# Performance work log

Hardware: AMD Instinct MI355X
Metric: run time of the kernel (lower is better)

Reference implementation:

```python
import jax, jax.numpy as jnp
import numpy as np

N, IN, HID, OUT = 8192, 512, 256, 128

def setup_inputs() -> dict:
    key = jax.random.key(0)
    k1, k2, k3, k4 = jax.random.split(key, 4)
    adj = jax.random.uniform(k1, (N, N), dtype=jnp.float32)
    feature = jax.random.normal(k2, (N, IN), dtype=jnp.float32)
    W1 = jax.random.normal(k3, (IN, HID), dtype=jnp.float32) * (1.0 / np.sqrt(IN))
    b1 = jnp.zeros((HID,), dtype=jnp.float32)
    W2 = jax.random.normal(k4, (HID, OUT), dtype=jnp.float32) * (1.0 / np.sqrt(HID))
    b2 = jnp.zeros((OUT,), dtype=jnp.float32)
    return {"adj": adj, "feature": feature, "W1": W1, "b1": b1, "W2": W2, "b2": b2}

def reference(adj, feature, W1, b1, W2, b2):
    # GCN encoder: layer1 (relu) then layer2 (linear output)
    h = jax.nn.relu(adj @ (feature @ W1) + b1)   # [N, HID]
    h = adj @ (h @ W2) + b2                      # [N, OUT]
    # InnerProductDecoder: sigmoid(flatten(h @ h.T))
    logits = h @ h.T                             # [N, N]
    h_noise = jax.nn.sigmoid(logits.reshape(-1)) # [N*N]
    return (h_noise, h)
```

## Files before the change

kernel.cpp:

```cpp
#include <hip/hip_runtime.h>


#define KSPLIT 8

typedef __bf16 bf16x8_t __attribute__((ext_vector_type(8)));
typedef __bf16 bf16x4_t __attribute__((ext_vector_type(4)));
typedef float  f32x4_t  __attribute__((ext_vector_type(4)));

#define MFMA_BF16(a, b, c) __builtin_amdgcn_mfma_f32_16x16x32_bf16((a), (b), (c), 0, 0, 0)

__device__ __forceinline__ bf16x8_t cvt8(float4 u, float4 v) {
    bf16x8_t o;
    o[0] = (__bf16)u.x; o[1] = (__bf16)u.y; o[2] = (__bf16)u.z; o[3] = (__bf16)u.w;
    o[4] = (__bf16)v.x; o[5] = (__bf16)v.y; o[6] = (__bf16)v.z; o[7] = (__bf16)v.w;
    return o;
}

__device__ __forceinline__ void gload_lds16(const void* g, void* l) {
    __builtin_amdgcn_global_load_lds(
        (const __attribute__((address_space(1))) unsigned int*)g,
        (__attribute__((address_space(3))) unsigned int*)l, 16, 0, 0);
}

__global__ __launch_bounds__(256) void cast_adj(
    const float* __restrict__ adj, __bf16* __restrict__ ab)
{
    const size_t j = (size_t)blockIdx.x * 256 + threadIdx.x;
    const float4* p = (const float4*)adj + j * 2;
    float4 u = p[0], v = p[1];
    *(bf16x8_t*)(ab + j * 8) = cvt8(u, v);
}

__global__ __launch_bounds__(256) void cast_all(
    const float* __restrict__ feat, const float* __restrict__ W1,
    const float* __restrict__ W2, __bf16* __restrict__ fb,
    __bf16* __restrict__ w1t, __bf16* __restrict__ w2t)
{
    const int j = blockIdx.x * 256 + threadIdx.x;
    if (j < 524288) {
        const float4* p = (const float4*)feat + (size_t)j * 2;
        float4 u = p[0], v = p[1];
        *(bf16x8_t*)(fb + (size_t)j * 8) = cvt8(u, v);
    } else if (j < 524288 + 131072) {
        int t = j - 524288;
        int k = t >> 8, n = t & 255;
        w1t[n * 512 + k] = (__bf16)W1[t];
    } else if (j < 524288 + 131072 + 32768) {
        int t = j - 655360;
        int k = t >> 7, n = t & 127;
        w2t[n * 256 + k] = (__bf16)W2[t];
    }
}

template<int MT, int WC>
__global__ __launch_bounds__(256, 2) void gemm_bt_cbf16(
    const __bf16* __restrict__ X, const __bf16* __restrict__ Yb,
    __bf16* __restrict__ C, int K, int N)
{
    constexpr int WR = 4 / WC;
    constexpr int BM = WR * MT * 16;
    constexpr int BN = WC * 64;
    const int mblk = blockIdx.x, nblk = blockIdx.y;
    const int w = threadIdx.x >> 6, lane = threadIdx.x & 63;
    const int wr = w / WC, wc = w % WC;
    const int q = lane >> 4, l16 = lane & 15;
    const int mbase = mblk * BM + wr * (MT * 16);
    const int nbase = nblk * BN + wc * 64;

    f32x4_t acc[MT][4];
    const f32x4_t z = {0.f, 0.f, 0.f, 0.f};
#pragma unroll
    for (int i = 0; i < MT; i++)
#pragma unroll
        for (int jj = 0; jj < 4; jj++) acc[i][jj] = z;

    const __bf16* Xr[MT];
    const __bf16* Yr[4];
#pragma unroll
    for (int i = 0; i < MT; i++) Xr[i] = X + (size_t)(mbase + i * 16 + l16) * K + q * 8;
#pragma unroll
    for (int jj = 0; jj < 4; jj++) Yr[jj] = Yb + (size_t)(nbase + jj * 16 + l16) * K + q * 8;

    for (int k = 0; k < K; k += 32) {
        bf16x8_t a[MT], b[4];
#pragma unroll
        for (int i = 0; i < MT; i++) a[i] = *(const bf16x8_t*)(Xr[i] + k);
#pragma unroll
        for (int jj = 0; jj < 4; jj++) b[jj] = *(const bf16x8_t*)(Yr[jj] + k);
#pragma unroll
        for (int i = 0; i < MT; i++)
#pragma unroll
            for (int jj = 0; jj < 4; jj++) acc[i][jj] = MFMA_BF16(a[i], b[jj], acc[i][jj]);
    }

#pragma unroll
    for (int i = 0; i < MT; i++)
#pragma unroll
        for (int jj = 0; jj < 4; jj++) {
            const int row0 = mbase + i * 16 + q * 4;
            const int col = nbase + jj * 16 + l16;
#pragma unroll
            for (int r = 0; r < 4; r++)
                C[(size_t)(row0 + r) * N + col] = (__bf16)acc[i][jj][r];
        }
}

template<int NN>
__global__ __launch_bounds__(256, 2) void gemm_adj_bf(
    const __bf16* __restrict__ A, const __bf16* __restrict__ Y,
    float* __restrict__ P, int kchunk)
{
    constexpr int NT = NN / 64;
    __shared__ __bf16 As[2][4096];

    const int mblk = blockIdx.x;
    const int ks = blockIdx.y;
    const int w = threadIdx.x >> 6, lane = threadIdx.x & 63;
    const int q = lane >> 4, l16 = lane & 15;
    const int kbase = ks * kchunk;
    const int ntiles = kchunk >> 6;

    const __bf16* gsrc[2];
    int loff[2];
#pragma unroll
    for (int j = 0; j < 2; j++) {
        const int row = j * 32 + w * 8 + (lane >> 3);
        const int gdst = lane & 7;
        const int gsrcg = gdst ^ (row & 7);
        gsrc[j] = A + (size_t)(mblk * 64 + row) * 8192 + kbase + gsrcg * 8;
        loff[j] = row * 64 + gdst * 8;
    }

    const __bf16* Yr[NT];
#pragma unroll
    for (int jj = 0; jj < NT; jj++)
        Yr[jj] = Y + (size_t)(w * (NN / 4) + jj * 16 + l16) * 8192 + q * 8;

    f32x4_t acc[4][NT];
    const f32x4_t z = {0.f, 0.f, 0.f, 0.f};
#pragma unroll
    for (int i = 0; i < 4; i++)
#pragma unroll
        for (int jj = 0; jj < NT; jj++) acc[i][jj] = z;

#pragma unroll
    for (int j = 0; j < 2; j++) gload_lds16(gsrc[j], &As[0][0] + loff[j]);

    int buf = 0;
    for (int kt = 0; kt < ntiles; kt++) {
        const int kk = kbase + (kt << 6);

        bf16x8_t breg[2][NT];
#pragma unroll
        for (int s = 0; s < 2; s++)
#pragma unroll
            for (int jj = 0; jj < NT; jj++)
                breg[s][jj] = *(const bf16x8_t*)(Yr[jj] + kk + s * 32);

        __syncthreads();

        if (kt + 1 < ntiles) {
            const int koff = (kt + 1) << 6;
#pragma unroll
            for (int j = 0; j < 2; j++)
                gload_lds16(gsrc[j] + koff, &As[buf ^ 1][0] + loff[j]);
        }

        const __bf16* __restrict__ L = &As[buf][0];
#pragma unroll
        for (int s = 0; s < 2; s++) {
            bf16x8_t a[4];
#pragma unroll
            for (int i = 0; i < 4; i++) {
                const int r = i * 16 + l16;
                const int g = ((s * 4 + q) ^ (r & 7)) * 8;
                a[i] = *(const bf16x8_t*)(L + r * 64 + g);
            }
#pragma unroll
            for (int i = 0; i < 4; i++)
#pragma unroll
                for (int jj = 0; jj < NT; jj++)
                    acc[i][jj] = MFMA_BF16(a[i], breg[s][jj], acc[i][jj]);
        }
        buf ^= 1;
    }

#pragma unroll
    for (int i = 0; i < 4; i++)
#pragma unroll
        for (int jj = 0; jj < NT; jj++) {
            const int row0 = mblk * 64 + i * 16 + q * 4;
            const int col = w * (NN / 4) + jj * 16 + l16;
            float* pp = P + ((size_t)ks * 8192 + row0) * NN + col;
#pragma unroll
            for (int r = 0; r < 4; r++) pp[(size_t)r * NN] = acc[i][jj][r];
        }
}

__global__ __launch_bounds__(256) void epi_relu_bias(
    const float* __restrict__ P, const float* __restrict__ bias,
    __bf16* __restrict__ H)
{
    const size_t SL = (size_t)8192 * 256;
    const size_t idx = ((size_t)blockIdx.x * 256 + threadIdx.x) * 4;
    float4 s;
    s.x = s.y = s.z = s.w = 0.f;
#pragma unroll
    for (int k = 0; k < KSPLIT; k++) {
        float4 t = *(const float4*)(P + k * SL + idx);
        s.x += t.x; s.y += t.y; s.z += t.z; s.w += t.w;
    }
    const int col = (int)(idx & 255);
    float4 bb = *(const float4*)(bias + col);
    bf16x4_t o;
    o[0] = (__bf16)fmaxf(s.x + bb.x, 0.f);
    o[1] = (__bf16)fmaxf(s.y + bb.y, 0.f);
    o[2] = (__bf16)fmaxf(s.z + bb.z, 0.f);
    o[3] = (__bf16)fmaxf(s.w + bb.w, 0.f);
    *(bf16x4_t*)(H + idx) = o;
}

__global__ __launch_bounds__(256) void epi_bias_out(
    const float* __restrict__ P, const float* __restrict__ bias,
    float* __restrict__ Hout, __bf16* __restrict__ Hbf)
{
    const size_t SL = (size_t)8192 * 128;
    const size_t idx = ((size_t)blockIdx.x * 256 + threadIdx.x) * 4;
    float4 s;
    s.x = s.y = s.z = s.w = 0.f;
#pragma unroll
    for (int k = 0; k < KSPLIT; k++) {
        float4 t = *(const float4*)(P + k * SL + idx);
        s.x += t.x; s.y += t.y; s.z += t.z; s.w += t.w;
    }
    const int col = (int)(idx & 127);
    float4 bb = *(const float4*)(bias + col);
    float4 o;
    o.x = s.x + bb.x; o.y = s.y + bb.y; o.z = s.z + bb.z; o.w = s.w + bb.w;
    *(float4*)(Hout + idx) = o;
    bf16x4_t ob;
    ob[0] = (__bf16)o.x; ob[1] = (__bf16)o.y; ob[2] = (__bf16)o.z; ob[3] = (__bf16)o.w;
    *(bf16x4_t*)(Hbf + idx) = ob;
}

__global__ __launch_bounds__(256, 2) void gemm_sig(
    const __bf16* __restrict__ H, float* __restrict__ out)
{
    const int mblk = blockIdx.x, nblk = blockIdx.y;
    const int w = threadIdx.x >> 6, lane = threadIdx.x & 63;
    const int wr = w >> 1, wc = w & 1;
    const int q = lane >> 4, l16 = lane & 15;
    const int mbase = mblk * 128 + wr * 64;
    const int nbase = nblk * 128 + wc * 64;

    f32x4_t acc[4][4];
    const f32x4_t z = {0.f, 0.f, 0.f, 0.f};
#pragma unroll
    for (int i = 0; i < 4; i++)
#pragma unroll
        for (int jj = 0; jj < 4; jj++) acc[i][jj] = z;

#pragma unroll
    for (int k = 0; k < 128; k += 32) {
        bf16x8_t a[4], b[4];
#pragma unroll
        for (int i = 0; i < 4; i++)
            a[i] = *(const bf16x8_t*)(H + (size_t)(mbase + i * 16 + l16) * 128 + k + q * 8);
#pragma unroll
        for (int jj = 0; jj < 4; jj++)
            b[jj] = *(const bf16x8_t*)(H + (size_t)(nbase + jj * 16 + l16) * 128 + k + q * 8);
#pragma unroll
        for (int i = 0; i < 4; i++)
#pragma unroll
            for (int jj = 0; jj < 4; jj++) acc[i][jj] = MFMA_BF16(a[i], b[jj], acc[i][jj]);
    }

#pragma unroll
    for (int i = 0; i < 4; i++)
#pragma unroll
        for (int jj = 0; jj < 4; jj++) {
            const int row0 = mbase + i * 16 + q * 4;
            const int col = nbase + jj * 16 + l16;
#pragma unroll
            for (int r = 0; r < 4; r++) {
                float x = acc[i][jj][r];
                out[(size_t)(row0 + r) * 8192 + col] = 1.0f / (1.0f + __expf(-x));
            }
        }
}

extern "C" void kernel_launch(void* const* d_in, const int* in_sizes, int n_in,
                              void* d_out, int out_size, void* d_ws, size_t ws_size,
                              hipStream_t stream)
{
    const float* adj  = (const float*)d_in[0];
    const float* feat = (const float*)d_in[1];
    const float* W1   = (const float*)d_in[2];
    const float* b1   = (const float*)d_in[3];
    const float* W2   = (const float*)d_in[4];
    const float* b2   = (const float*)d_in[5];
    float* out = (float*)d_out;

    char* p = (char*)d_ws;
    __bf16* adjbf  = (__bf16*)p; p += (size_t)8192 * 8192 * 2;
    __bf16* featbf = (__bf16*)p; p += (size_t)8192 * 512 * 2;
    __bf16* W1T    = (__bf16*)p; p += (size_t)256 * 512 * 2;
    __bf16* W2T    = (__bf16*)p; p += (size_t)128 * 256 * 2;
    __bf16* t1T    = (__bf16*)p; p += (size_t)256 * 8192 * 2;
    __bf16* h1     = (__bf16*)p; p += (size_t)8192 * 256 * 2;
    __bf16* t2T    = (__bf16*)p; p += (size_t)128 * 8192 * 2;
    __bf16* hbf    = (__bf16*)p; p += (size_t)8192 * 128 * 2;
    float* part    = (float*)p;

    cast_adj<<<32768, 256, 0, stream>>>(adj, adjbf);
    cast_all<<<2688, 256, 0, stream>>>(feat, W1, W2, featbf, W1T, W2T);
    gemm_bt_cbf16<2, 2><<<dim3(4, 64), 256, 0, stream>>>(W1T, featbf, t1T, 512, 8192);
    gemm_adj_bf<256><<<dim3(128, KSPLIT), 256, 0, stream>>>(adjbf, t1T, part, 8192 / KSPLIT);
    epi_relu_bias<<<2048, 256, 0, stream>>>(part, b1, h1);
    gemm_bt_cbf16<1, 2><<<dim3(4, 64), 256, 0, stream>>>(W2T, h1, t2T, 256, 8192);
    gemm_adj_bf<128><<<dim3(128, KSPLIT), 256, 0, stream>>>(adjbf, t2T, part, 8192 / KSPLIT);
    epi_bias_out<<<1024, 256, 0, stream>>>(part, b2, out + (size_t)8192 * 8192, hbf);
    gemm_sig<<<dim3(64, 64), 256, 0, stream>>>(hbf, out);
}
```

Measured before the change: 691.2 us.

## Retile adjacency GEMM to 128x128 blocks with both operands staged in LDS

Replaces the adjacency-times-features GEMM with a 128x128 output tile per block. Both A and B are now loaded into double-buffered swizzled LDS via direct global-to-LDS loads, instead of each wave reading B straight from global memory into registers. The split-K factor changes per layer (4 for the 256-wide layer, 8 for the 128-wide one), and the epilogue reduction counts are adjusted to match. The goal is more operand reuse per block and less redundant global traffic for B, at the cost of more LDS per block and fewer blocks in the grid.

New measurement: 650.3 us. 1.06x faster.

```diff
diff --git a/kernel.cpp b/kernel.cpp
--- a/kernel.cpp
+++ b/kernel.cpp
@@ -1,7 +1,5 @@
 #include <hip/hip_runtime.h>
 
-
-#define KSPLIT 8
 
 typedef __bf16 bf16x8_t __attribute__((ext_vector_type(8)));
 typedef __bf16 bf16x4_t __attribute__((ext_vector_type(4)));
@@ -106,81 +104,84 @@
 }
 
 template<int NN>
-__global__ __launch_bounds__(256, 2) void gemm_adj_bf(
+__global__ __launch_bounds__(256, 2) void gemm_adj_m97(
     const __bf16* __restrict__ A, const __bf16* __restrict__ Y,
     float* __restrict__ P, int kchunk)
 {
-    constexpr int NT = NN / 64;
-    __shared__ __bf16 As[2][4096];
+    __shared__ __bf16 As[2][8192];
+    __shared__ __bf16 Bs[2][8192];
 
     const int mblk = blockIdx.x;
-    const int ks = blockIdx.y;
+    const int nblk = blockIdx.y;
+    const int ks   = blockIdx.z;
     const int w = threadIdx.x >> 6, lane = threadIdx.x & 63;
+    const int wr = w >> 1, wc = w & 1;
     const int q = lane >> 4, l16 = lane & 15;
     const int kbase = ks * kchunk;
     const int ntiles = kchunk >> 6;
 
-    const __bf16* gsrc[2];
-    int loff[2];
-#pragma unroll
-    for (int j = 0; j < 2; j++) {
-        const int row = j * 32 + w * 8 + (lane >> 3);
-        const int gdst = lane & 7;
-        const int gsrcg = gdst ^ (row & 7);
-        gsrc[j] = A + (size_t)(mblk * 64 + row) * 8192 + kbase + gsrcg * 8;
-        loff[j] = row * 64 + gdst * 8;
-    }
-
-    const __bf16* Yr[NT];
-#pragma unroll
-    for (int jj = 0; jj < NT; jj++)
-        Yr[jj] = Y + (size_t)(w * (NN / 4) + jj * 16 + l16) * 8192 + q * 8;
-
-    f32x4_t acc[4][NT];
+    const int srow = lane >> 3;
+    const int gdst = lane & 7;
+    const __bf16* gA[4];
+    const __bf16* gB[4];
+    int lofs[4];
+#pragma unroll
+    for (int j = 0; j < 4; j++) {
+        const int row = (w * 4 + j) * 8 + srow;
+        const int gs = gdst ^ (row & 7);
+        gA[j] = A + (size_t)(mblk * 128 + row) * 8192 + kbase + gs * 8;
+        gB[j] = Y + (size_t)(nblk * 128 + row) * 8192 + kbase + gs * 8;
+        lofs[j] = row * 64 + gdst * 8;
+    }
+
+    f32x4_t acc[4][4];
     const f32x4_t z = {0.f, 0.f, 0.f, 0.f};
 #pragma unroll
     for (int i = 0; i < 4; i++)
 #pragma unroll
-        for (int jj = 0; jj < NT; jj++) acc[i][jj] = z;
-
-#pragma unroll
-    for (int j = 0; j < 2; j++) gload_lds16(gsrc[j], &As[0][0] + loff[j]);
+        for (int jj = 0; jj < 4; jj++) acc[i][jj] = z;
+
+#pragma unroll
+    for (int j = 0; j < 4; j++) {
+        gload_lds16(gA[j], &As[0][0] + lofs[j]);
+        gload_lds16(gB[j], &Bs[0][0] + lofs[j]);
+    }
 
     int buf = 0;
     for (int kt = 0; kt < ntiles; kt++) {
-        const int kk = kbase + (kt << 6);
-
-        bf16x8_t breg[2][NT];
-#pragma unroll
-        for (int s = 0; s < 2; s++)
-#pragma unroll
-            for (int jj = 0; jj < NT; jj++)
-                breg[s][jj] = *(const bf16x8_t*)(Yr[jj] + kk + s * 32);
-
         __syncthreads();
 
         if (kt + 1 < ntiles) {
             const int koff = (kt + 1) << 6;
 #pragma unroll
-            for (int j = 0; j < 2; j++)
-                gload_lds16(gsrc[j] + koff, &As[buf ^ 1][0] + loff[j]);
-        }
-
-        const __bf16* __restrict__ L = &As[buf][0];
+            for (int j = 0; j < 4; j++) {
+                gload_lds16(gA[j] + koff, &As[buf ^ 1][0] + lofs[j]);
+                gload_lds16(gB[j] + koff, &Bs[buf ^ 1][0] + lofs[j]);
+            }
+        }
+
+        const __bf16* __restrict__ LA = &As[buf][0];
+        const __bf16* __restrict__ LB = &Bs[buf][0];
 #pragma unroll
         for (int s = 0; s < 2; s++) {
-            bf16x8_t a[4];
+            bf16x8_t a[4], b[4];
 #pragma unroll
             for (int i = 0; i < 4; i++) {
-                const int r = i * 16 + l16;
+                const int r = wr * 64 + i * 16 + l16;
                 const int g = ((s * 4 + q) ^ (r & 7)) * 8;
-                a[i] = *(const bf16x8_t*)(L + r * 64 + g);
+                a[i] = *(const bf16x8_t*)(LA + r * 64 + g);
             }
 #pragma unroll
+            for (int jj = 0; jj < 4; jj++) {
+                const int r = wc * 64 + jj * 16 + l16;
+                const int g = ((s * 4 + q) ^ (r & 7)) * 8;
+                b[jj] = *(const bf16x8_t*)(LB + r * 64 + g);
+            }
+#pragma unroll
             for (int i = 0; i < 4; i++)
 #pragma unroll
-                for (int jj = 0; jj < NT; jj++)
-                    acc[i][jj] = MFMA_BF16(a[i], breg[s][jj], acc[i][jj]);
+                for (int jj = 0; jj < 4; jj++)
+                    acc[i][jj] = MFMA_BF16(a[i], b[jj], acc[i][jj]);
         }
         buf ^= 1;
     }
@@ -188,9 +189,9 @@
 #pragma unroll
     for (int i = 0; i < 4; i++)
 #pragma unroll
-        for (int jj = 0; jj < NT; jj++) {
-            const int row0 = mblk * 64 + i * 16 + q * 4;
-            const int col = w * (NN / 4) + jj * 16 + l16;
+        for (int jj = 0; jj < 4; jj++) {
+            const int row0 = mblk * 128 + wr * 64 + i * 16 + q * 4;
+            const int col = nblk * 128 + wc * 64 + jj * 16 + l16;
             float* pp = P + ((size_t)ks * 8192 + row0) * NN + col;
 #pragma unroll
             for (int r = 0; r < 4; r++) pp[(size_t)r * NN] = acc[i][jj][r];
@@ -206,7 +207,7 @@
     float4 s;
     s.x = s.y = s.z = s.w = 0.f;
 #pragma unroll
-    for (int k = 0; k < KSPLIT; k++) {
+    for (int k = 0; k < 4; k++) {
         float4 t = *(const float4*)(P + k * SL + idx);
         s.x += t.x; s.y += t.y; s.z += t.z; s.w += t.w;
     }
@@ -229,7 +230,7 @@
     float4 s;
     s.x = s.y = s.z = s.w = 0.f;
 #pragma unroll
-    for (int k = 0; k < KSPLIT; k++) {
+    for (int k = 0; k < 8; k++) {
         float4 t = *(const float4*)(P + k * SL + idx);
         s.x += t.x; s.y += t.y; s.z += t.z; s.w += t.w;
     }
@@ -315,10 +316,10 @@
     cast_adj<<<32768, 256, 0, stream>>>(adj, adjbf);
     cast_all<<<2688, 256, 0, stream>>>(feat, W1, W2, featbf, W1T, W2T);
     gemm_bt_cbf16<2, 2><<<dim3(4, 64), 256, 0, stream>>>(W1T, featbf, t1T, 512, 8192);
-    gemm_adj_bf<256><<<dim3(128, KSPLIT), 256, 0, stream>>>(adjbf, t1T, part, 8192 / KSPLIT);
+    gemm_adj_m97<256><<<dim3(64, 2, 4), 256, 0, stream>>>(adjbf, t1T, part, 2048);
     epi_relu_bias<<<2048, 256, 0, stream>>>(part, b1, h1);
     gemm_bt_cbf16<1, 2><<<dim3(4, 64), 256, 0, stream>>>(W2T, h1, t2T, 256, 8192);
-    gemm_adj_bf<128><<<dim3(128, KSPLIT), 256, 0, stream>>>(adjbf, t2T, part, 8192 / KSPLIT);
+    gemm_adj_m97<128><<<dim3(64, 1, 8), 256, 0, stream>>>(adjbf, t2T, part, 1024);
     epi_bias_out<<<1024, 256, 0, stream>>>(part, b2, out + (size_t)8192 * 8192, hbf);
     gemm_sig<<<dim3(64, 64), 256, 0, stream>>>(hbf, out);
 }
```
